# Performance work log

Measured on AMD Instinct MI355X. Metric: run time of the kernel, lower is better.

Reference implementation:

```python
import jax, jax.numpy as jnp
import numpy as np
from math import sqrt

B, H, L, E = 2, 16, 1024, 64
MEM, LMEM = 896, 128
KV = L + MEM + LMEM  # 2048


def rel_shift(x):
    # Transformer-XL relative shift. x: [B,H,i,j] -> [B,H,i,j]
    b, h, i, j = x.shape
    x = jnp.pad(x, ((0, 0), (0, 0), (0, 0), (0, i)))  # [B,H,i,i+j]
    l = i + j - 1
    x = x.reshape(b, h, -1)
    pad = (-x.shape[-1]) % l
    x = jnp.pad(x, ((0, 0), (0, 0), (0, pad))).reshape(b, h, -1, l)
    return x[..., :i, i - 1:]


def setup_inputs() -> dict:
    key = jax.random.key(0)
    kq, kk, kv_, kp = jax.random.split(key, 4)
    return {
        "q": jax.random.normal(kq, (B, H, L, E), jnp.float32),
        "k": jax.random.normal(kk, (B, H, KV, E), jnp.float32),
        "v": jax.random.normal(kv_, (B, H, KV, E), jnp.float32),
        "attn_mask": jnp.ones((B, L), bool),
        "pos_emb": jax.random.normal(kp, (H, KV, E), jnp.float32),
        "kv_len": KV,
        "mem_len": MEM,
        "lmem_len": LMEM,
    }


def reference(q, k, v, attn_mask, pos_emb, kv_len, mem_len, lmem_len):
    b, h, l, e = q.shape
    scale = 1.0 / sqrt(e)
    dots = jnp.einsum('bhid,bhjd->bhij', q, k) * scale  # [B,H,L,KV]
    mask_value = -jnp.finfo(dots.dtype).max

    # relative position bias
    pos = pos_emb[:, -kv_len:].astype(q.dtype)  # [H,KV,E]
    pos_dots = jnp.einsum('bhid,hjd->bhij', q, pos) * scale
    pos_dots = rel_shift(pos_dots)
    left = dots.shape[-1] - pos_dots.shape[-1]
    pos_dots = jnp.pad(pos_dots, ((0, 0), (0, 0), (0, 0), (left, 0)))
    dots = dots + pos_dots

    total_mem = mem_len + lmem_len
    # padding mask
    m = attn_mask[:, None, :, None] & attn_mask[:, None, None, :]  # [B,1,L,L]
    m = jnp.pad(m, ((0, 0), (0, 0), (0, 0), (total_mem, 0)), constant_values=True)
    dots = jnp.where(m, dots, mask_value)
    # causal mask (memory positions always visible)
    causal = jnp.triu(jnp.ones((l, l + total_mem), bool), k=1 + total_mem)
    dots = jnp.where(causal[None, None], mask_value, dots)

    attn = jax.nn.softmax(dots, axis=-1)  # dropout in eval mode -> identity
    out = jnp.einsum('bhij,bhjd->bhid', attn, v)
    return out.transpose(0, 2, 1, 3).reshape(b, l, h * e)
```

## Files before the change

### kernel.cpp

```cpp
#include <hip/hip_runtime.h>
#include <stdint.h>


typedef __attribute__((ext_vector_type(4))) float f32x4;
typedef __attribute__((ext_vector_type(8))) short s16x8;
typedef __attribute__((ext_vector_type(2))) unsigned int u32x2;
typedef unsigned short ushort_t;

#define L_Q 1024
#define NKV 2048
#define TM  1024
#define NPOS 2176

#define WS_K   0
#define WS_VT  4194304
#define WS_POS 8388608
#define WS_TOTAL_USHORT 10616832
#define WS_NEED_BYTES (WS_TOTAL_USHORT * 2)

#define QS_CONST (0.125f * 1.44269504088896340736f)

__device__ __forceinline__ void mfma16(f32x4& c, s16x8 a, s16x8 b) {
  asm("v_mfma_f32_16x16x32_bf16 %0, %1, %2, %0" : "+v"(c) : "v"(a), "v"(b));
}

__device__ __forceinline__ float exp2_(float x) {
#if __has_builtin(__builtin_amdgcn_exp2f)
  return __builtin_amdgcn_exp2f(x);
#else
  float r; asm("v_exp_f32 %0, %1" : "=v"(r) : "v"(x)); return r;
#endif
}

__device__ __forceinline__ ushort_t f2bf(float f) {
  union { float f; unsigned int u; } v; v.f = f;
  unsigned int u = v.u;
  return (ushort_t)((u + 0x7FFFu + ((u >> 16) & 1u)) >> 16);
}

__device__ __forceinline__ void gl_lds16(const ushort_t* g, ushort_t* l) {
  __builtin_amdgcn_global_load_lds(
      (const __attribute__((address_space(1))) unsigned int*)g,
      (__attribute__((address_space(3))) unsigned int*)l, 16, 0, 0);
}

__device__ __forceinline__ s16x8 ldfrag(const ushort_t* base, int row, int chunk) {
  int idx = (row * 64 + chunk * 8) ^ ((row & 7) << 3);
  return *(const s16x8*)(base + idx);
}


#define NK_U 524288
#define NP_U 278528
#define LIN_TOTAL 802816

__global__ __launch_bounds__(256) void prep_lin(
    const float* __restrict__ k, const float* __restrict__ pos,
    ushort_t* __restrict__ ws)
{
  int u = blockIdx.x * 256 + threadIdx.x;
  if (u >= LIN_TOTAL) return;
  if (u < NK_U) {
    int bh = u >> 14, rem = u & 16383;
    int j = rem >> 3, db = (rem & 7) << 3;
    size_t off = (((size_t)(bh << 11) + j) << 6);
    f32x4 a = *(const f32x4*)(k + off + db);
    f32x4 b = *(const f32x4*)(k + off + db + 4);
    s16x8 o;
    o[0] = (short)f2bf(a[0]); o[1] = (short)f2bf(a[1]);
    o[2] = (short)f2bf(a[2]); o[3] = (short)f2bf(a[3]);
    o[4] = (short)f2bf(b[0]); o[5] = (short)f2bf(b[1]);
    o[6] = (short)f2bf(b[2]); o[7] = (short)f2bf(b[3]);
    *(s16x8*)(ws + WS_K + off + (db ^ ((j & 7) << 3))) = o;
  } else {
    int t = u - NK_U;
    int h = t / 17408;
    int rem = t - h * 17408;
    int p = rem >> 3, db = (rem & 7) << 3;
    s16x8 o;
    if (p < 2048) {
      size_t off = (((size_t)(h << 11) + p) << 6) + db;
      f32x4 a = *(const f32x4*)(pos + off);
      f32x4 b = *(const f32x4*)(pos + off + 4);
      o[0] = (short)f2bf(a[0]); o[1] = (short)f2bf(a[1]);
      o[2] = (short)f2bf(a[2]); o[3] = (short)f2bf(a[3]);
      o[4] = (short)f2bf(b[0]); o[5] = (short)f2bf(b[1]);
      o[6] = (short)f2bf(b[2]); o[7] = (short)f2bf(b[3]);
    } else {
      for (int e = 0; e < 8; ++e) o[e] = 0;
    }
    *(s16x8*)(ws + WS_POS + (size_t)h * (NPOS * 64) + p * 64 + (db ^ ((p & 7) << 3))) = o;
  }
}

__global__ __launch_bounds__(256) void prep_vt(
    const float* __restrict__ v, ushort_t* __restrict__ ws)
{
  int u = blockIdx.x * 256 + threadIdx.x;
  int bh = u >> 12, rem = u & 4095;
  int tile = rem >> 7, r2 = rem & 127;
  int jl = r2 >> 3, db = (r2 & 7) << 3;
  int j0 = tile << 6;
  ushort_t vals[4][8];
#pragma unroll
  for (int m = 0; m < 4; ++m) {
    size_t off = (((size_t)(bh << 11) + j0 + jl + 16 * m) << 6) + db;
    f32x4 a = *(const f32x4*)(v + off);
    f32x4 b = *(const f32x4*)(v + off + 4);
    vals[m][0] = f2bf(a[0]); vals[m][1] = f2bf(a[1]);
    vals[m][2] = f2bf(a[2]); vals[m][3] = f2bf(a[3]);
    vals[m][4] = f2bf(b[0]); vals[m][5] = f2bf(b[1]);
    vals[m][6] = f2bf(b[2]); vals[m][7] = f2bf(b[3]);
  }
  ushort_t* vt = ws + WS_VT;
#pragma unroll
  for (int e = 0; e < 8; ++e) {
    int d = db + e;
    int cpos = (jl << 2) ^ ((d & 7) << 3);
    union { ushort_t s[4]; u32x2 w; } pk;
    pk.s[0] = vals[0][e]; pk.s[1] = vals[1][e];
    pk.s[2] = vals[2][e]; pk.s[3] = vals[3][e];
    *(u32x2*)(vt + (((size_t)(bh << 6) + d) << 11) + j0 + cpos) = pk.w;
  }
}


__global__ __launch_bounds__(256, 2) void memattn_fast(
    const float* __restrict__ q, const ushort_t* __restrict__ ws,
    float* __restrict__ out)
{
  __shared__ __align__(16) ushort_t sK[2][64 * 64];
  __shared__ __align__(16) ushort_t sV[2][64 * 64];
  __shared__ __align__(16) ushort_t sPos[2][128 * 64];
  __shared__ __align__(16) ushort_t sPl[4 * 16 * 72];

  const int tid = threadIdx.x;
  const int lane = tid & 63;
  const int w = tid >> 6;
  const int bid = blockIdx.x;
  const int bh = bid & 31;
  const int raw = bid >> 5;
  const int ib = (raw < 8) ? raw : 23 - raw;
  const int h = bh & 15;
  const int b = bh >> 4;
  const int i0 = ib * 64;
  const int iw0 = i0 + w * 16;
  const int jc = lane & 15;
  const int g = lane >> 4;

  const ushort_t* kb = ws + WS_K + (size_t)bh * (NKV * 64);
  const ushort_t* vtb = ws + WS_VT + (size_t)bh * (64 * NKV);
  const ushort_t* pb = ws + WS_POS + (size_t)h * (NPOS * 64);

  s16x8 qf[2];
  {
    const float* qr = q + (size_t)bh * (L_Q * 64) + (size_t)(iw0 + jc) * 64 + g * 8;
#pragma unroll
    for (int c = 0; c < 2; ++c) {
      f32x4 a = *(const f32x4*)(qr + 32 * c);
      f32x4 b2 = *(const f32x4*)(qr + 32 * c + 4);
      s16x8 f;
      f[0] = (short)f2bf(a[0] * QS_CONST); f[1] = (short)f2bf(a[1] * QS_CONST);
      f[2] = (short)f2bf(a[2] * QS_CONST); f[3] = (short)f2bf(a[3] * QS_CONST);
      f[4] = (short)f2bf(b2[0] * QS_CONST); f[5] = (short)f2bf(b2[1] * QS_CONST);
      f[6] = (short)f2bf(b2[2] * QS_CONST); f[7] = (short)f2bf(b2[3] * QS_CONST);
      qf[c] = f;
    }
  }

  f32x4 m4, l4, acc[4];
#pragma unroll
  for (int r = 0; r < 4; ++r) { m4[r] = -1e30f; l4[r] = 0.f; }
#pragma unroll
  for (int d = 0; d < 4; ++d) { f32x4 z = {0.f, 0.f, 0.f, 0.f}; acc[d] = z; }

  int srcl[4]; int lof[4];
#pragma unroll
  for (int reg = 0; reg < 4; ++reg) {
    int r = 4 * g + reg;
    int sc = jc + 15 - r;
    srcl[reg] = (lane & 48) | (sc & 15);
    lof[reg] = (sc < 16);
  }

  const int nsteps = ib + 17;
  const int lrow8 = lane >> 3;
  const int lc8 = (lane & 7) * 8;

  auto STAGE = [&](int buf, int st) {
    const int j0 = st * 64;
    const int pwb = j0 - i0 + 960;
#pragma unroll
    for (int c2 = 0; c2 < 2; ++c2) {
      int c = 2 * w + c2;
      gl_lds16(kb + (size_t)(j0 + c * 8 + lrow8) * 64 + lc8, &sK[buf][c * 512]);
    }
#pragma unroll
    for (int c2 = 0; c2 < 2; ++c2) {
      int c = 2 * w + c2;
      gl_lds16(vtb + (size_t)(c * 8 + lrow8) * NKV + j0 + lc8, &sV[buf][c * 512]);
    }
#pragma unroll
    for (int c2 = 0; c2 < 4; ++c2) {
      int c = 4 * w + c2;
      gl_lds16(pb + (size_t)(pwb + c * 8 + lrow8) * 64 + lc8, &sPos[buf][c * 512]);
    }
  };

  STAGE(0, 0);
  asm volatile("s_waitcnt vmcnt(0)" ::: "memory");
  __syncthreads();
  int cur = 0;

  for (int st = 0; st < nsteps; ++st) {
    const int j0 = st * 64;
    if (st + 1 < nsteps) STAGE(cur ^ 1, st + 1);

    f32x4 s4[4];
#pragma unroll
    for (int t = 0; t < 4; ++t) {
      f32x4 z = {0.f, 0.f, 0.f, 0.f};
      s4[t] = z;
#pragma unroll
      for (int c = 0; c < 2; ++c)
        mfma16(s4[t], qf[c], ldfrag(sK[cur], 16 * t + jc, g + 4 * c));
    }
    f32x4 pd[5];
#pragma unroll
    for (int t = 0; t < 5; ++t) {
      f32x4 z = {0.f, 0.f, 0.f, 0.f};
      pd[t] = z;
      int lr = 48 - 16 * w + 16 * t + jc;
#pragma unroll
      for (int c = 0; c < 2; ++c)
        mfma16(pd[t], qf[c], ldfrag(sPos[cur], lr, g + 4 * c));
    }
#pragma unroll
    for (int reg = 0; reg < 4; ++reg) {
      float sh0 = __shfl(pd[0][reg], srcl[reg], 64);
      float sh1 = __shfl(pd[1][reg], srcl[reg], 64);
      float sh2 = __shfl(pd[2][reg], srcl[reg], 64);
      float sh3 = __shfl(pd[3][reg], srcl[reg], 64);
      float sh4 = __shfl(pd[4][reg], srcl[reg], 64);
      s4[0][reg] += lof[reg] ? sh0 : sh1;
      s4[1][reg] += lof[reg] ? sh1 : sh2;
      s4[2][reg] += lof[reg] ? sh2 : sh3;
      s4[3][reg] += lof[reg] ? sh3 : sh4;
    }
    if (j0 + 63 - iw0 > TM) {
#pragma unroll
      for (int t = 0; t < 4; ++t)
#pragma unroll
        for (int reg = 0; reg < 4; ++reg) {
          int j = j0 + 16 * t + jc;
          int i = iw0 + 4 * g + reg;
          if (j - i > TM) s4[t][reg] = -1e30f;
        }
    }
    f32x4 ps[4];
#pragma unroll
    for (int reg = 0; reg < 4; ++reg) {
      float mx = fmaxf(fmaxf(s4[0][reg], s4[1][reg]), fmaxf(s4[2][reg], s4[3][reg]));
      mx = fmaxf(mx, __shfl_xor(mx, 1, 16));
      mx = fmaxf(mx, __shfl_xor(mx, 2, 16));
      mx = fmaxf(mx, __shfl_xor(mx, 4, 16));
      mx = fmaxf(mx, __shfl_xor(mx, 8, 16));
      float mold = m4[reg];
      float mnew = fmaxf(mold, mx);
      float sf = exp2_(mold - mnew);
      m4[reg] = mnew;
      float rs = 0.f;
#pragma unroll
      for (int t = 0; t < 4; ++t) {
        float pv = exp2_(s4[t][reg] - mnew);
        ps[t][reg] = pv;
        rs += pv;
      }
      l4[reg] = l4[reg] * sf + rs;
#pragma unroll
      for (int d = 0; d < 4; ++d) acc[d][reg] *= sf;
    }
#pragma unroll
    for (int reg = 0; reg < 4; ++reg) {
      int r = 4 * g + reg;
      unsigned int lo = (unsigned int)f2bf(ps[0][reg]) | ((unsigned int)f2bf(ps[1][reg]) << 16);
      unsigned int hi = (unsigned int)f2bf(ps[2][reg]) | ((unsigned int)f2bf(ps[3][reg]) << 16);
      u32x2 pk2 = {lo, hi};
      *(u32x2*)(sPl + (w * 16 + r) * 72 + jc * 4) = pk2;
    }
    asm volatile("s_waitcnt lgkmcnt(0)" ::: "memory");
#pragma unroll
    for (int kk = 0; kk < 2; ++kk) {
      s16x8 pa = *(const s16x8*)(sPl + (w * 16 + jc) * 72 + 8 * g + 32 * kk);
#pragma unroll
      for (int d = 0; d < 4; ++d)
        mfma16(acc[d], pa, ldfrag(sV[cur], 16 * d + jc, g + 4 * kk));
    }
    asm volatile("s_waitcnt vmcnt(0)" ::: "memory");
    __syncthreads();
    cur ^= 1;
  }

#pragma unroll
  for (int reg = 0; reg < 4; ++reg) {
    float lv = l4[reg];
    lv += __shfl_xor(lv, 1, 16);
    lv += __shfl_xor(lv, 2, 16);
    lv += __shfl_xor(lv, 4, 16);
    lv += __shfl_xor(lv, 8, 16);
    float rinv = 1.0f / lv;
    int i = iw0 + 4 * g + reg;
#pragma unroll
    for (int d = 0; d < 4; ++d) {
      int col = h * 64 + 16 * d + jc;
      out[(size_t)(b * L_Q + i) * 1024 + col] = acc[d][reg] * rinv;
    }
  }
}


__global__ __launch_bounds__(512, 1) void memattn_fallback(
    const float* __restrict__ q, const float* __restrict__ k,
    const float* __restrict__ v, const float* __restrict__ pos,
    float* __restrict__ out)
{
  __shared__ __align__(16) ushort_t sK[64 * 64];
  __shared__ __align__(16) ushort_t sV[64 * 64];
  __shared__ __align__(16) ushort_t sP[256 * 64];
  __shared__ __align__(16) ushort_t sPl[8 * 16 * 72];

  const int tid = threadIdx.x;
  const int lane = tid & 63;
  const int w = tid >> 6;
  const int bid = blockIdx.x;
  const int bh = bid & 31;
  const int ib = bid >> 5;
  const int h = bh & 15;
  const int b = bh >> 4;
  const int i0 = ib * 128;
  const int iw0 = i0 + w * 16;
  const int jc = lane & 15;
  const int g = lane >> 4;

  const float* qb = q + (size_t)bh * L_Q * 64;
  const float* kb = k + (size_t)bh * NKV * 64;
  const float* vb = v + (size_t)bh * NKV * 64;
  const float* pb = pos + (size_t)h * NKV * 64;

  s16x8 qf[2];
  {
    const float* qr = qb + (size_t)(iw0 + jc) * 64 + g * 8;
#pragma unroll
    for (int c = 0; c < 2; ++c) {
      f32x4 a = *(const f32x4*)(qr + 32 * c);
      f32x4 b2 = *(const f32x4*)(qr + 32 * c + 4);
      s16x8 f;
      f[0] = (short)f2bf(a[0] * QS_CONST); f[1] = (short)f2bf(a[1] * QS_CONST);
      f[2] = (short)f2bf(a[2] * QS_CONST); f[3] = (short)f2bf(a[3] * QS_CONST);
      f[4] = (short)f2bf(b2[0] * QS_CONST); f[5] = (short)f2bf(b2[1] * QS_CONST);
      f[6] = (short)f2bf(b2[2] * QS_CONST); f[7] = (short)f2bf(b2[3] * QS_CONST);
      qf[c] = f;
    }
  }

  f32x4 m4, l4, acc[4];
#pragma unroll
  for (int r = 0; r < 4; ++r) { m4[r] = -1e30f; l4[r] = 0.f; }
#pragma unroll
  for (int d = 0; d < 4; ++d) { f32x4 z = {0.f, 0.f, 0.f, 0.f}; acc[d] = z; }

  int srcl[4]; int lof[4];
#pragma unroll
  for (int reg = 0; reg < 4; ++reg) {
    int r = 4 * g + reg;
    int sc = jc + 15 - r;
    srcl[reg] = (lane & 48) | (sc & 15);
    lof[reg] = (sc < 16);
  }

  const int limit = iw0 + 15 + TM;
  const int nsteps = i0 / 64 + 18;
  int staged_hi = 0;

  const int srow = tid >> 3;
  const int c8 = (tid & 7) * 8;

  for (int st = 0; st < nsteps; ++st) {
    const int j0 = st * 64;
    __syncthreads();

    {
      const float* kr = kb + (size_t)(j0 + srow) * 64 + c8;
      f32x4 a = *(const f32x4*)(kr);
      f32x4 b2 = *(const f32x4*)(kr + 4);
      s16x8 fk;
      fk[0] = (short)f2bf(a[0]);  fk[1] = (short)f2bf(a[1]);
      fk[2] = (short)f2bf(a[2]);  fk[3] = (short)f2bf(a[3]);
      fk[4] = (short)f2bf(b2[0]); fk[5] = (short)f2bf(b2[1]);
      fk[6] = (short)f2bf(b2[2]); fk[7] = (short)f2bf(b2[3]);
      int idx = (srow * 64 + c8) ^ ((srow & 7) << 3);
      *(s16x8*)(sK + idx) = fk;

      const float* vr = vb + (size_t)(j0 + srow) * 64 + c8;
      f32x4 va = *(const f32x4*)(vr);
      f32x4 vb2 = *(const f32x4*)(vr + 4);
      float vals[8] = {va[0], va[1], va[2], va[3], vb2[0], vb2[1], vb2[2], vb2[3]};
      int pj = (srow & 15) * 4 + (srow >> 4);
#pragma unroll
      for (int e = 0; e < 8; ++e) {
        int d = c8 + e;
        int vidx = (d * 64 + pj) ^ ((d & 7) << 3);
        sV[vidx] = f2bf(vals[e]);
      }
    }
    {
      int p_lo = (st == 0) ? (896 - i0) : staged_hi;
      int cnt = (st == 0) ? 192 : 64;
      for (int ro = srow; ro < cnt; ro += 64) {
        int p = p_lo + ro;
        int pg = p < 2047 ? p : 2047;
        const float* pr = pb + (size_t)pg * 64 + c8;
        f32x4 a = *(const f32x4*)(pr);
        f32x4 b2 = *(const f32x4*)(pr + 4);
        s16x8 fp;
        fp[0] = (short)f2bf(a[0]);  fp[1] = (short)f2bf(a[1]);
        fp[2] = (short)f2bf(a[2]);  fp[3] = (short)f2bf(a[3]);
        fp[4] = (short)f2bf(b2[0]); fp[5] = (short)f2bf(b2[1]);
        fp[6] = (short)f2bf(b2[2]); fp[7] = (short)f2bf(b2[3]);
        int rr = p & 255;
        int idx = (rr * 64 + c8) ^ ((rr & 7) << 3);
        *(s16x8*)(sP + idx) = fp;
      }
      staged_hi = p_lo + cnt;
    }
    __syncthreads();

    if (j0 > limit) continue;

    f32x4 s4[4];
#pragma unroll
    for (int t = 0; t < 4; ++t) {
      f32x4 z = {0.f, 0.f, 0.f, 0.f};
      s4[t] = z;
#pragma unroll
      for (int c = 0; c < 2; ++c)
        mfma16(s4[t], qf[c], ldfrag(sK, 16 * t + jc, g + 4 * c));
    }
    const int pw0 = j0 - iw0 + 1008;
    f32x4 pd[5];
#pragma unroll
    for (int t = 0; t < 5; ++t) {
      f32x4 z = {0.f, 0.f, 0.f, 0.f};
      pd[t] = z;
      int prow = (pw0 + 16 * t + jc) & 255;
#pragma unroll
      for (int c = 0; c < 2; ++c)
        mfma16(pd[t], qf[c], ldfrag(sP, prow, g + 4 * c));
    }
#pragma unroll
    for (int t = 0; t < 4; ++t) {
#pragma unroll
      for (int reg = 0; reg < 4; ++reg) {
        float a0 = __shfl(pd[t][reg], srcl[reg], 64);
        float a1 = __shfl(pd[t + 1][reg], srcl[reg], 64);
        s4[t][reg] += lof[reg] ? a0 : a1;
      }
    }
    if (j0 + 63 - iw0 > TM) {
#pragma unroll
      for (int t = 0; t < 4; ++t)
#pragma unroll
        for (int reg = 0; reg < 4; ++reg) {
          int j = j0 + 16 * t + jc;
          int i = iw0 + 4 * g + reg;
          if (j - i > TM) s4[t][reg] = -1e30f;
        }
    }
    f32x4 ps[4];
#pragma unroll
    for (int reg = 0; reg < 4; ++reg) {
      float mx = fmaxf(fmaxf(s4[0][reg], s4[1][reg]), fmaxf(s4[2][reg], s4[3][reg]));
      mx = fmaxf(mx, __shfl_xor(mx, 1, 16));
      mx = fmaxf(mx, __shfl_xor(mx, 2, 16));
      mx = fmaxf(mx, __shfl_xor(mx, 4, 16));
      mx = fmaxf(mx, __shfl_xor(mx, 8, 16));
      float mold = m4[reg];
      float mnew = fmaxf(mold, mx);
      float sf = exp2_(mold - mnew);
      m4[reg] = mnew;
      float rs = 0.f;
#pragma unroll
      for (int t = 0; t < 4; ++t) {
        float pv = exp2_(s4[t][reg] - mnew);
        ps[t][reg] = pv;
        rs += pv;
      }
      l4[reg] = l4[reg] * sf + rs;
#pragma unroll
      for (int d = 0; d < 4; ++d) acc[d][reg] *= sf;
    }
#pragma unroll
    for (int reg = 0; reg < 4; ++reg) {
      int r = 4 * g + reg;
      unsigned int lo = (unsigned int)f2bf(ps[0][reg]) | ((unsigned int)f2bf(ps[1][reg]) << 16);
      unsigned int hi = (unsigned int)f2bf(ps[2][reg]) | ((unsigned int)f2bf(ps[3][reg]) << 16);
      u32x2 pk2 = {lo, hi};
      *(u32x2*)(sPl + (w * 16 + r) * 72 + jc * 4) = pk2;
    }
    asm volatile("s_waitcnt lgkmcnt(0)" ::: "memory");
#pragma unroll
    for (int kk = 0; kk < 2; ++kk) {
      s16x8 pa = *(const s16x8*)(sPl + (w * 16 + jc) * 72 + 8 * g + 32 * kk);
#pragma unroll
      for (int d = 0; d < 4; ++d)
        mfma16(acc[d], pa, ldfrag(sV, 16 * d + jc, g + 4 * kk));
    }
  }

#pragma unroll
  for (int reg = 0; reg < 4; ++reg) {
    float lv = l4[reg];
    lv += __shfl_xor(lv, 1, 16);
    lv += __shfl_xor(lv, 2, 16);
    lv += __shfl_xor(lv, 4, 16);
    lv += __shfl_xor(lv, 8, 16);
    float rinv = 1.0f / lv;
    int i = iw0 + 4 * g + reg;
#pragma unroll
    for (int d = 0; d < 4; ++d) {
      int col = h * 64 + 16 * d + jc;
      out[(size_t)(b * L_Q + i) * 1024 + col] = acc[d][reg] * rinv;
    }
  }
}

extern "C" void kernel_launch(void* const* d_in, const int* in_sizes, int n_in,
                              void* d_out, int out_size, void* d_ws, size_t ws_size,
                              hipStream_t stream) {
  (void)in_sizes; (void)n_in; (void)out_size;
  const float* q = (const float*)d_in[0];
  const float* k = (const float*)d_in[1];
  const float* v = (const float*)d_in[2];
  const float* pos = (const float*)d_in[4];
  float* out = (float*)d_out;

  if (ws_size >= (size_t)WS_NEED_BYTES) {
    ushort_t* ws = (ushort_t*)d_ws;
    hipLaunchKernelGGL(prep_lin, dim3((LIN_TOTAL + 255) / 256), dim3(256), 0, stream,
                       k, pos, ws);
    hipLaunchKernelGGL(prep_vt, dim3(512), dim3(256), 0, stream, v, ws);
    hipLaunchKernelGGL(memattn_fast, dim3(512), dim3(256), 0, stream, q, ws, out);
  } else {
    hipLaunchKernelGGL(memattn_fallback, dim3(256), dim3(512), 0, stream,
                       q, k, v, pos, out);
  }
}
```

Before: 86.72 us.

## Use ring buffer for pos-emb tiles and load V fragments directly from global

Replaces the double-buffered 128-row positional-embedding staging with a 192-row circular LDS ring, so each step loads only the 64 new rows instead of re-fetching the overlapping window. V^T fragments are now read straight from global memory into registers instead of being staged through LDS, which removes the sV buffers and the XOR swizzle in the V transpose prep. This cuts global-to-LDS traffic and LDS footprint, which may allow higher occupancy. The cost is that direct global V loads may add latency on the critical path.

Result: slower. 101.6 us (+17.2%).

```diff
diff --git a/kernel.cpp b/kernel.cpp
--- a/kernel.cpp
+++ b/kernel.cpp
@@ -116,7 +116,7 @@
 #pragma unroll
   for (int e = 0; e < 8; ++e) {
     int d = db + e;
-    int cpos = (jl << 2) ^ ((d & 7) << 3);
+    int cpos = (jl << 2);
     union { ushort_t s[4]; u32x2 w; } pk;
     pk.s[0] = vals[0][e]; pk.s[1] = vals[1][e];
     pk.s[2] = vals[2][e]; pk.s[3] = vals[3][e];
@@ -130,8 +130,7 @@
     float* __restrict__ out)
 {
   __shared__ __align__(16) ushort_t sK[2][64 * 64];
-  __shared__ __align__(16) ushort_t sV[2][64 * 64];
-  __shared__ __align__(16) ushort_t sPos[2][128 * 64];
+  __shared__ __align__(16) ushort_t sPos[192 * 64];
   __shared__ __align__(16) ushort_t sPl[4 * 16 * 72];
 
   const int tid = threadIdx.x;
@@ -186,35 +185,52 @@
   const int nsteps = ib + 17;
   const int lrow8 = lane >> 3;
   const int lc8 = (lane & 7) * 8;
-
-  auto STAGE = [&](int buf, int st) {
+  const int B0 = 960 - i0;
+
+  auto STAGE_K = [&](int buf, int st) {
     const int j0 = st * 64;
-    const int pwb = j0 - i0 + 960;
 #pragma unroll
     for (int c2 = 0; c2 < 2; ++c2) {
       int c = 2 * w + c2;
       gl_lds16(kb + (size_t)(j0 + c * 8 + lrow8) * 64 + lc8, &sK[buf][c * 512]);
     }
+  };
+  auto STAGE_P = [&](int st, int rb) {
+    const int abs0 = B0 + st * 64 + 128;
 #pragma unroll
     for (int c2 = 0; c2 < 2; ++c2) {
       int c = 2 * w + c2;
-      gl_lds16(vtb + (size_t)(c * 8 + lrow8) * NKV + j0 + lc8, &sV[buf][c * 512]);
-    }
-#pragma unroll
-    for (int c2 = 0; c2 < 4; ++c2) {
-      int c = 4 * w + c2;
-      gl_lds16(pb + (size_t)(pwb + c * 8 + lrow8) * 64 + lc8, &sPos[buf][c * 512]);
+      int rdest = rb + 128 + c * 8;
+      if (rdest >= 192) rdest -= 192;
+      gl_lds16(pb + (size_t)(abs0 + c * 8 + lrow8) * 64 + lc8, &sPos[rdest * 64]);
     }
   };
 
-  STAGE(0, 0);
+  int rb = B0 % 192;
+  STAGE_K(0, 0);
+#pragma unroll
+  for (int c2 = 0; c2 < 4; ++c2) {
+    int c = 4 * w + c2;
+    int rdest = rb + c * 8;
+    if (rdest >= 192) rdest -= 192;
+    gl_lds16(pb + (size_t)(B0 + c * 8 + lrow8) * 64 + lc8, &sPos[rdest * 64]);
+  }
   asm volatile("s_waitcnt vmcnt(0)" ::: "memory");
   __syncthreads();
   int cur = 0;
 
   for (int st = 0; st < nsteps; ++st) {
     const int j0 = st * 64;
-    if (st + 1 < nsteps) STAGE(cur ^ 1, st + 1);
+    if (st + 1 < nsteps) {
+      STAGE_K(cur ^ 1, st + 1);
+      STAGE_P(st, rb);
+    }
+    s16x8 vf[4][2];
+#pragma unroll
+    for (int d = 0; d < 4; ++d)
+#pragma unroll
+      for (int kk = 0; kk < 2; ++kk)
+        vf[d][kk] = *(const s16x8*)(vtb + (size_t)(16 * d + jc) * NKV + j0 + 8 * (g + 4 * kk));
 
     f32x4 s4[4];
 #pragma unroll
@@ -230,10 +246,11 @@
     for (int t = 0; t < 5; ++t) {
       f32x4 z = {0.f, 0.f, 0.f, 0.f};
       pd[t] = z;
-      int lr = 48 - 16 * w + 16 * t + jc;
+      int rr = rb + 48 - 16 * w + 16 * t + jc;
+      if (rr >= 192) rr -= 192;
 #pragma unroll
       for (int c = 0; c < 2; ++c)
-        mfma16(pd[t], qf[c], ldfrag(sPos[cur], lr, g + 4 * c));
+        mfma16(pd[t], qf[c], ldfrag(sPos, rr, g + 4 * c));
     }
 #pragma unroll
     for (int reg = 0; reg < 4; ++reg) {
@@ -294,11 +311,12 @@
       s16x8 pa = *(const s16x8*)(sPl + (w * 16 + jc) * 72 + 8 * g + 32 * kk);
 #pragma unroll
       for (int d = 0; d < 4; ++d)
-        mfma16(acc[d], pa, ldfrag(sV[cur], 16 * d + jc, g + 4 * kk));
+        mfma16(acc[d], pa, vf[d][kk]);
     }
     asm volatile("s_waitcnt vmcnt(0)" ::: "memory");
     __syncthreads();
     cur ^= 1;
+    rb += 64; if (rb >= 192) rb -= 192;
   }
 
 #pragma unroll
```
